# Performance work log

Hardware: AMD Instinct MI355X
Metric: run time of the kernel (lower is better)

The kernel has to match this reference:

```python
import jax, jax.numpy as jnp
import numpy as np

B, T, C, H = 4, 4096, 1024, 16

def setup_inputs() -> dict:
    key = jax.random.key(0)
    k1, k2, k3, k4 = jax.random.split(key, 4)
    return {
        "x": jax.random.normal(k1, (B, T, C), dtype=jnp.float32),
        "W_attn": jax.random.normal(k2, (C, C), dtype=jnp.float32) * 0.02,
        "b_attn": jnp.zeros((C,), dtype=jnp.float32),
        "W_proj": jax.random.normal(k3, (C, C), dtype=jnp.float32) * 0.02,
        "b_proj": jnp.zeros((C,), dtype=jnp.float32),
        "temp": jnp.ones((H, 1), dtype=jnp.float32),
        "n_head": H,
    }

def reference(x, W_attn, b_attn, W_proj, b_proj, temp, n_head):
    Bb, Tt, Cc = x.shape
    D = Cc // n_head
    # c_attn (torch Linear: x @ W.T + b)
    w = x @ W_attn.T + b_attn                         # (B,T,C)
    w = w.reshape(Bb, Tt, n_head, D).transpose(0, 2, 1, 3)  # (B,H,T,D)
    # F.normalize over token axis (dim=-2), eps=1e-12
    norm = jnp.maximum(jnp.sqrt(jnp.sum(w * w, axis=-2, keepdims=True)), 1e-12)
    w_normed = w / norm
    tmp = jnp.sum(w_normed ** 2, axis=-1) * temp      # (B,H,T) * (H,1) -> (B,H,T)
    Pi = jax.nn.softmax(tmp, axis=1)                  # softmax over heads
    Pi_prob = Pi / (jnp.sum(Pi, axis=-1, keepdims=True) + 1e-8)  # (B,H,T)
    dots = jnp.einsum('bht,bhtd->bhd', Pi_prob, w ** 2)          # (B,H,D)
    attn = 1.0 / (1.0 + dots)                         # (B,H,D)
    y = -(w * Pi[..., None]) * attn[:, :, None, :]    # (B,H,T,D)
    y = y.transpose(0, 2, 1, 3).reshape(Bb, Tt, Cc)
    return y @ W_proj.T + b_proj
```

## Files before the change

### kernel.cpp

```cpp
#include <hip/hip_runtime.h>
#include <hip/hip_bf16.h>

#define BB 4
#define TT 4096
#define CC 1024
#define HH 16
#define DD 64

typedef __attribute__((ext_vector_type(8))) short short8;
typedef __attribute__((ext_vector_type(8))) __bf16 bf16x8;
typedef __attribute__((ext_vector_type(4))) float f32x4;

static __device__ __forceinline__ unsigned short f2bf(float f) {
    unsigned int u = __builtin_bit_cast(unsigned int, f);
    unsigned int r = (u + 0x7FFFu + ((u >> 16) & 1u)) >> 16;
    return (unsigned short)r;
}
static __device__ __forceinline__ float bf2f(unsigned short h) {
    return __builtin_bit_cast(float, ((unsigned int)h) << 16);
}

__global__ void k_f32_to_bf16(const float* __restrict__ src,
                              unsigned short* __restrict__ dst, int n4) {
    int i = blockIdx.x * 256 + threadIdx.x;
    if (i >= n4) return;
    float4 v = ((const float4*)src)[i];
    ushort4 o;
    o.x = f2bf(v.x); o.y = f2bf(v.y); o.z = f2bf(v.z); o.w = f2bf(v.w);
    ((ushort4*)dst)[i] = o;
}

#define GBM 256
#define GBN 256
#define GBK 32

static __device__ __forceinline__ void stage_tile32(
    const unsigned short* __restrict__ Gbase, unsigned short* lbase,
    int k0, int K, int wave, int lane)
{
    #pragma unroll
    for (int q = 0; q < 2; ++q) {
        int c = (wave * 2 + q) * 64 + lane;
        int r = c >> 2;
        int j = c & 3;
        int srcj = (j - (r >> 1)) & 3;
        const unsigned short* g = Gbase + (size_t)r * K + k0 + srcj * 8;
        __builtin_amdgcn_global_load_lds(
            (const __attribute__((address_space(1))) void*)g,
            (__attribute__((address_space(3))) void*)(lbase + (wave * 2 + q) * 512),
            16, 0, 0);
    }
}

template<int MODE>
__global__ __launch_bounds__(512, 2)
void k_gemm256(const unsigned short* __restrict__ A,
               const unsigned short* __restrict__ B,
               const float* __restrict__ bias,
               void* __restrict__ Cout,
               float* __restrict__ S,
               int M, int N, int K)
{
    __shared__ unsigned short lds[4][16384];
    const int tid  = threadIdx.x;
    const int wave = tid >> 6;
    const int lane = tid & 63;
    const int wr = wave >> 2;
    const int wc = wave & 3;
    const int fr = lane & 15;
    const int hi = lane >> 4;

    const int wg  = blockIdx.x;
    const int swz = (wg & 7) * 32 + (wg >> 3);
    const int bn  = swz & 3;
    const int bm  = swz >> 2;

    const unsigned short* Abase = A + (size_t)(bm * GBM) * K;
    const unsigned short* Bbase = B + (size_t)(bn * GBN) * K;

    const int nt = K / GBK;

    const int sl   = (hi + (fr >> 1)) & 3;
    const int aoff = (wr * 128 + fr) * 32 + sl * 8;
    const int boff = 8192 + (wc * 64 + fr) * 32 + sl * 8;

    f32x4 acc[8][4] = {};

    stage_tile32(Abase, lds[0],        0,       K, wave, lane);
    stage_tile32(Bbase, lds[0] + 8192, 0,       K, wave, lane);
    stage_tile32(Abase, lds[1],        GBK,     K, wave, lane);
    stage_tile32(Bbase, lds[1] + 8192, GBK,     K, wave, lane);
    stage_tile32(Abase, lds[2],        2 * GBK, K, wave, lane);
    stage_tile32(Bbase, lds[2] + 8192, 2 * GBK, K, wave, lane);
    asm volatile("s_waitcnt vmcnt(8)" ::: "memory");
    __builtin_amdgcn_s_barrier();

    for (int kt = 0; kt < nt; ++kt) {
        const unsigned short* buf = lds[kt & 3];
        unsigned short* sbuf = lds[(kt + 3) & 3];
        int k3 = kt + 3; if (k3 >= nt) k3 = nt - 1;

        short8 af0[4], bf0[4];
        #pragma unroll
        for (int i = 0; i < 4; ++i) af0[i] = *(const short8*)&buf[aoff + i * 512];
        #pragma unroll
        for (int i = 0; i < 4; ++i) bf0[i] = *(const short8*)&buf[boff + i * 512];
        stage_tile32(Abase, sbuf, k3 * GBK, K, wave, lane);
        __builtin_amdgcn_s_barrier();
        asm volatile("s_waitcnt lgkmcnt(0)" ::: "memory");
        __builtin_amdgcn_s_setprio(1);
        #pragma unroll
        for (int mi = 0; mi < 4; ++mi)
            #pragma unroll
            for (int ni = 0; ni < 4; ++ni)
                acc[mi][ni] = __builtin_amdgcn_mfma_f32_16x16x32_bf16(
                    __builtin_bit_cast(bf16x8, af0[mi]),
                    __builtin_bit_cast(bf16x8, bf0[ni]),
                    acc[mi][ni], 0, 0, 0);
        __builtin_amdgcn_s_setprio(0);
        __builtin_amdgcn_s_barrier();

        short8 af1[4], bf1[4];
        #pragma unroll
        for (int i = 0; i < 4; ++i) af1[i] = *(const short8*)&buf[aoff + (4 + i) * 512];
        #pragma unroll
        for (int i = 0; i < 4; ++i) bf1[i] = *(const short8*)&buf[boff + i * 512];
        stage_tile32(Bbase, sbuf + 8192, k3 * GBK, K, wave, lane);
        asm volatile("s_waitcnt vmcnt(8)" ::: "memory");
        __builtin_amdgcn_s_barrier();
        asm volatile("s_waitcnt lgkmcnt(0)" ::: "memory");
        __builtin_amdgcn_s_setprio(1);
        #pragma unroll
        for (int mi = 0; mi < 4; ++mi)
            #pragma unroll
            for (int ni = 0; ni < 4; ++ni)
                acc[4 + mi][ni] = __builtin_amdgcn_mfma_f32_16x16x32_bf16(
                    __builtin_bit_cast(bf16x8, af1[mi]),
                    __builtin_bit_cast(bf16x8, bf1[ni]),
                    acc[4 + mi][ni], 0, 0, 0);
        __builtin_amdgcn_s_setprio(0);
        __builtin_amdgcn_s_barrier();
    }

    __syncthreads();

    const int cg = fr;
    const int rg = hi * 4;
    float* sblk = (float*)&lds[0][0];
    if (MODE == 0) {
        if (tid < GBN) sblk[tid] = 0.f;
        __syncthreads();
    }
    float csum[4] = {};
    #pragma unroll
    for (int mi = 0; mi < 8; ++mi) {
        #pragma unroll
        for (int ni = 0; ni < 4; ++ni) {
            int col = bn * GBN + wc * 64 + ni * 16 + cg;
            float bv = bias[col];
            #pragma unroll
            for (int j = 0; j < 4; ++j) {
                int row = bm * GBM + wr * 128 + mi * 16 + rg + j;
                float v = acc[mi][ni][j] + bv;
                if (MODE == 0) {
                    ((unsigned short*)Cout)[(size_t)row * N + col] = f2bf(v);
                    csum[ni] += v * v;
                } else {
                    ((float*)Cout)[(size_t)row * N + col] = v;
                }
            }
        }
    }
    if (MODE == 0) {
        #pragma unroll
        for (int ni = 0; ni < 4; ++ni)
            atomicAdd(&sblk[wc * 64 + ni * 16 + cg], csum[ni]);
        __syncthreads();
        const int b = bm >> 4;
        if (tid < GBN) atomicAdd(&S[b * CC + bn * GBN + tid], sblk[tid]);
    }
}

__global__ __launch_bounds__(256)
void k_row_softmax(const unsigned short* __restrict__ w16, const float* __restrict__ S,
                   const float* __restrict__ temp,
                   float* __restrict__ Pi, float* __restrict__ dotsU,
                   float* __restrict__ sumPi)
{
    __shared__ float dots_local[CC];
    __shared__ float sPi_local[HH];
    const int tid  = threadIdx.x;
    const int wave = tid >> 6;
    const int lane = tid & 63;
    const int bb   = blockIdx.x >> 7;
    const int tile = blockIdx.x & 127;

    for (int c = tid; c < CC; c += 256) dots_local[c] = 0.f;
    if (tid < HH) sPi_local[tid] = 0.f;
    __syncthreads();

    const int g3 = lane >> 3;
    const int li = lane & 7;

    float inv[2][8], tsc[2];
    #pragma unroll
    for (int q = 0; q < 2; ++q) {
        int c = q * 512 + lane * 8;
        const float4* sp = (const float4*)&S[bb * CC + c];
        float4 s0 = sp[0], s1 = sp[1];
        inv[q][0] = 1.f / fmaxf(s0.x, 1e-24f); inv[q][1] = 1.f / fmaxf(s0.y, 1e-24f);
        inv[q][2] = 1.f / fmaxf(s0.z, 1e-24f); inv[q][3] = 1.f / fmaxf(s0.w, 1e-24f);
        inv[q][4] = 1.f / fmaxf(s1.x, 1e-24f); inv[q][5] = 1.f / fmaxf(s1.y, 1e-24f);
        inv[q][6] = 1.f / fmaxf(s1.z, 1e-24f); inv[q][7] = 1.f / fmaxf(s1.w, 1e-24f);
        tsc[q] = temp[q * 8 + g3];
    }

    float dacc[2][8] = {};
    float sPiAcc[2] = {};

    for (int i = 0; i < 8; ++i) {
        int t = tile * 32 + wave * 8 + i;
        const unsigned short* row = w16 + ((size_t)bb * TT + t) * CC;
        float wf[2][8];
        float pq[2];
        #pragma unroll
        for (int q = 0; q < 2; ++q) {
            short8 v = *(const short8*)&row[q * 512 + lane * 8];
            float s = 0.f;
            #pragma unroll
            for (int j = 0; j < 8; ++j) {
                wf[q][j] = bf2f((unsigned short)v[j]);
                s += wf[q][j] * wf[q][j] * inv[q][j];
            }
            pq[q] = s;
        }
        #pragma unroll
        for (int off = 1; off < 8; off <<= 1) {
            pq[0] += __shfl_xor(pq[0], off);
            pq[1] += __shfl_xor(pq[1], off);
        }
        pq[0] *= tsc[0]; pq[1] *= tsc[1];
        float mx = fmaxf(pq[0], pq[1]);
        mx = fmaxf(mx, __shfl_xor(mx, 8));
        mx = fmaxf(mx, __shfl_xor(mx, 16));
        mx = fmaxf(mx, __shfl_xor(mx, 32));
        float e0 = __expf(pq[0] - mx), e1 = __expf(pq[1] - mx);
        float ss = e0 + e1;
        ss += __shfl_xor(ss, 8);
        ss += __shfl_xor(ss, 16);
        ss += __shfl_xor(ss, 32);
        float rs = 1.f / ss;
        float piv[2] = { e0 * rs, e1 * rs };
        #pragma unroll
        for (int q = 0; q < 2; ++q) {
            #pragma unroll
            for (int j = 0; j < 8; ++j)
                dacc[q][j] += piv[q] * wf[q][j] * wf[q][j];
            if (li == 0) {
                Pi[((size_t)(bb * HH + q * 8 + g3)) * TT + t] = piv[q];
                sPiAcc[q] += piv[q];
            }
        }
    }

    #pragma unroll
    for (int q = 0; q < 2; ++q) {
        int c = q * 512 + lane * 8;
        #pragma unroll
        for (int j = 0; j < 8; ++j)
            atomicAdd(&dots_local[c + j], dacc[q][j]);
        if (li == 0) atomicAdd(&sPi_local[q * 8 + g3], sPiAcc[q]);
    }
    __syncthreads();
    for (int c = tid; c < CC; c += 256) atomicAdd(&dotsU[bb * CC + c], dots_local[c]);
    if (tid < HH) atomicAdd(&sumPi[bb * HH + tid], sPi_local[tid]);
}

__global__ void k_attnscale(const float* __restrict__ dotsU,
                            const float* __restrict__ sumPi,
                            float* __restrict__ attnScale) {
    int i = blockIdx.x * 256 + threadIdx.x;
    if (i >= BB * CC) return;
    int b = i >> 10;
    int h = (i >> 6) & 15;
    float sp = sumPi[b * HH + h] + 1e-8f;
    attnScale[i] = 1.f / (1.f + dotsU[i] / sp);
}

__global__ void k_make_y(unsigned short* __restrict__ wy, const float* __restrict__ Pi,
                         const float* __restrict__ attnScale)
{
    size_t i = (size_t)blockIdx.x * 256 + threadIdx.x;
    size_t flat = i * 8;
    int c = (int)(flat & (CC - 1));
    size_t bt = flat >> 10;
    int t = (int)(bt & (TT - 1));
    int b = (int)(bt >> 12);
    int h = c >> 6;
    float pi = Pi[((size_t)(b * HH + h)) * TT + t];
    short8 wv = *(const short8*)&wy[flat];
    f32x4 a0 = *(const f32x4*)&attnScale[b * CC + c];
    f32x4 a1 = *(const f32x4*)&attnScale[b * CC + c + 4];
    short8 o;
    #pragma unroll
    for (int j = 0; j < 4; ++j) {
        o[j]     = (short)f2bf(-(bf2f((unsigned short)wv[j])     * pi) * a0[j]);
        o[4 + j] = (short)f2bf(-(bf2f((unsigned short)wv[4 + j]) * pi) * a1[j]);
    }
    *(short8*)&wy[flat] = o;
}

extern "C" void kernel_launch(void* const* d_in, const int* in_sizes, int n_in,
                              void* d_out, int out_size, void* d_ws, size_t ws_size,
                              hipStream_t stream) {
    const float* x      = (const float*)d_in[0];
    const float* W_attn = (const float*)d_in[1];
    const float* b_attn = (const float*)d_in[2];
    const float* W_proj = (const float*)d_in[3];
    const float* b_proj = (const float*)d_in[4];
    const float* temp   = (const float*)d_in[5];

    unsigned short* xb = (unsigned short*)d_out;

    char* ws = (char*)d_ws;
    unsigned short* w16  = (unsigned short*)(ws);
    unsigned short* Wa16 = (unsigned short*)(ws + 33554432);
    unsigned short* Wp16 = (unsigned short*)(ws + 35651584);
    float* Pi        = (float*)(ws + 37748736);
    float* S         = (float*)(ws + 38797312);
    float* dotsU     = (float*)(ws + 38813696);
    float* sumPi     = (float*)(ws + 38830080);
    float* attnScale = (float*)(ws + 38830336);

    k_f32_to_bf16<<<dim3(16384), dim3(256), 0, stream>>>(x, xb, 4194304);
    k_f32_to_bf16<<<dim3(1024), dim3(256), 0, stream>>>(W_attn, Wa16, 262144);
    k_f32_to_bf16<<<dim3(1024), dim3(256), 0, stream>>>(W_proj, Wp16, 262144);

    hipMemsetAsync(S, 0, 16384 + 16384 + 256, stream);

    k_gemm256<0><<<dim3(256), dim3(512), 0, stream>>>(
        xb, Wa16, b_attn, w16, S, BB * TT, CC, CC);

    k_row_softmax<<<dim3(512), dim3(256), 0, stream>>>(w16, S, temp, Pi, dotsU, sumPi);

    k_attnscale<<<dim3(16), dim3(256), 0, stream>>>(dotsU, sumPi, attnScale);

    k_make_y<<<dim3(8192), dim3(256), 0, stream>>>(w16, Pi, attnScale);

    k_gemm256<1><<<dim3(256), dim3(512), 0, stream>>>(
        w16, Wp16, b_proj, d_out, nullptr, BB * TT, CC, CC);
}
```

Baseline: 142.8 us.

## Fold per-batch attention scale into projection weights and emit y in softmax pass

The per-(batch, channel) attention scale is folded into per-batch bf16 copies of W_proj, and the row-softmax kernel writes -w*Pi directly over w16. This removes the separate attnscale and make_y passes, the Pi buffer, and one full read/write sweep of the activation tensor. The projection GEMM now picks its batch's weight slice, which adds a small weight-scaling kernel and a larger weight workspace. The GEMM also drops a redundant second LDS load of the B fragments and reuses bf0.

```diff
diff --git a/kernel.cpp b/kernel.cpp
--- a/kernel.cpp
+++ b/kernel.cpp
@@ -74,9 +74,11 @@
     const int swz = (wg & 7) * 32 + (wg >> 3);
     const int bn  = swz & 3;
     const int bm  = swz >> 2;
+    const int b   = bm >> 4;
 
     const unsigned short* Abase = A + (size_t)(bm * GBM) * K;
-    const unsigned short* Bbase = B + (size_t)(bn * GBN) * K;
+    const unsigned short* Bbase = B +
+        ((size_t)((MODE == 1 ? b * N : 0) + bn * GBN)) * K;
 
     const int nt = K / GBK;
 
@@ -120,11 +122,9 @@
         __builtin_amdgcn_s_setprio(0);
         __builtin_amdgcn_s_barrier();
 
-        short8 af1[4], bf1[4];
+        short8 af1[4];
         #pragma unroll
         for (int i = 0; i < 4; ++i) af1[i] = *(const short8*)&buf[aoff + (4 + i) * 512];
-        #pragma unroll
-        for (int i = 0; i < 4; ++i) bf1[i] = *(const short8*)&buf[boff + i * 512];
         stage_tile32(Bbase, sbuf + 8192, k3 * GBK, K, wave, lane);
         asm volatile("s_waitcnt vmcnt(8)" ::: "memory");
         __builtin_amdgcn_s_barrier();
@@ -136,7 +136,7 @@
             for (int ni = 0; ni < 4; ++ni)
                 acc[4 + mi][ni] = __builtin_amdgcn_mfma_f32_16x16x32_bf16(
                     __builtin_bit_cast(bf16x8, af1[mi]),
-                    __builtin_bit_cast(bf16x8, bf1[ni]),
+                    __builtin_bit_cast(bf16x8, bf0[ni]),
                     acc[4 + mi][ni], 0, 0, 0);
         __builtin_amdgcn_s_setprio(0);
         __builtin_amdgcn_s_barrier();
@@ -176,16 +176,14 @@
         for (int ni = 0; ni < 4; ++ni)
             atomicAdd(&sblk[wc * 64 + ni * 16 + cg], csum[ni]);
         __syncthreads();
-        const int b = bm >> 4;
         if (tid < GBN) atomicAdd(&S[b * CC + bn * GBN + tid], sblk[tid]);
     }
 }
 
 __global__ __launch_bounds__(256)
-void k_row_softmax(const unsigned short* __restrict__ w16, const float* __restrict__ S,
+void k_row_softmax(unsigned short* __restrict__ w16, const float* __restrict__ S,
                    const float* __restrict__ temp,
-                   float* __restrict__ Pi, float* __restrict__ dotsU,
-                   float* __restrict__ sumPi)
+                   float* __restrict__ dotsU, float* __restrict__ sumPi)
 {
     __shared__ float dots_local[CC];
     __shared__ float sPi_local[HH];
@@ -220,7 +218,7 @@
 
     for (int i = 0; i < 8; ++i) {
         int t = tile * 32 + wave * 8 + i;
-        const unsigned short* row = w16 + ((size_t)bb * TT + t) * CC;
+        unsigned short* row = w16 + ((size_t)bb * TT + t) * CC;
         float wf[2][8];
         float pq[2];
         #pragma unroll
@@ -253,13 +251,14 @@
         float piv[2] = { e0 * rs, e1 * rs };
         #pragma unroll
         for (int q = 0; q < 2; ++q) {
-            #pragma unroll
-            for (int j = 0; j < 8; ++j)
+            short8 yo;
+            #pragma unroll
+            for (int j = 0; j < 8; ++j) {
                 dacc[q][j] += piv[q] * wf[q][j] * wf[q][j];
-            if (li == 0) {
-                Pi[((size_t)(bb * HH + q * 8 + g3)) * TT + t] = piv[q];
-                sPiAcc[q] += piv[q];
+                yo[j] = (short)f2bf(-wf[q][j] * piv[q]);
             }
+            *(short8*)&row[q * 512 + lane * 8] = yo;
+            if (li == 0) sPiAcc[q] += piv[q];
         }
     }
 
@@ -276,38 +275,27 @@
     if (tid < HH) atomicAdd(&sumPi[bb * HH + tid], sPi_local[tid]);
 }
 
-__global__ void k_attnscale(const float* __restrict__ dotsU,
-                            const float* __restrict__ sumPi,
-                            float* __restrict__ attnScale) {
+__global__ void k_scale_wproj(const float* __restrict__ Wp,
+                              const float* __restrict__ dotsU,
+                              const float* __restrict__ sumPi,
+                              unsigned short* __restrict__ out)
+{
     int i = blockIdx.x * 256 + threadIdx.x;
-    if (i >= BB * CC) return;
-    int b = i >> 10;
-    int h = (i >> 6) & 15;
-    float sp = sumPi[b * HH + h] + 1e-8f;
-    attnScale[i] = 1.f / (1.f + dotsU[i] / sp);
-}
-
-__global__ void k_make_y(unsigned short* __restrict__ wy, const float* __restrict__ Pi,
-                         const float* __restrict__ attnScale)
-{
-    size_t i = (size_t)blockIdx.x * 256 + threadIdx.x;
-    size_t flat = i * 8;
-    int c = (int)(flat & (CC - 1));
-    size_t bt = flat >> 10;
-    int t = (int)(bt & (TT - 1));
-    int b = (int)(bt >> 12);
-    int h = c >> 6;
-    float pi = Pi[((size_t)(b * HH + h)) * TT + t];
-    short8 wv = *(const short8*)&wy[flat];
-    f32x4 a0 = *(const f32x4*)&attnScale[b * CC + c];
-    f32x4 a1 = *(const f32x4*)&attnScale[b * CC + c + 4];
-    short8 o;
-    #pragma unroll
-    for (int j = 0; j < 4; ++j) {
-        o[j]     = (short)f2bf(-(bf2f((unsigned short)wv[j])     * pi) * a0[j]);
-        o[4 + j] = (short)f2bf(-(bf2f((unsigned short)wv[4 + j]) * pi) * a1[j]);
-    }
-    *(short8*)&wy[flat] = o;
+    int bq  = i >> 18;
+    int rem = i & 262143;
+    int n   = rem >> 8;
+    int cg  = (rem & 255) * 4;
+    float4 wv = *(const float4*)&Wp[n * CC + cg];
+    float4 du = *(const float4*)&dotsU[bq * CC + cg];
+    float sp = sumPi[bq * HH + (cg >> 6)] + 1e-8f;
+    float a0 = 1.f / (1.f + du.x / sp);
+    float a1 = 1.f / (1.f + du.y / sp);
+    float a2 = 1.f / (1.f + du.z / sp);
+    float a3 = 1.f / (1.f + du.w / sp);
+    ushort4 o;
+    o.x = f2bf(wv.x * a0); o.y = f2bf(wv.y * a1);
+    o.z = f2bf(wv.z * a2); o.w = f2bf(wv.w * a3);
+    *(ushort4*)&out[((size_t)bq * CC + n) * CC + cg] = o;
 }
 
 extern "C" void kernel_launch(void* const* d_in, const int* in_sizes, int n_in,
@@ -323,30 +311,25 @@
     unsigned short* xb = (unsigned short*)d_out;
 
     char* ws = (char*)d_ws;
-    unsigned short* w16  = (unsigned short*)(ws);
-    unsigned short* Wa16 = (unsigned short*)(ws + 33554432);
-    unsigned short* Wp16 = (unsigned short*)(ws + 35651584);
-    float* Pi        = (float*)(ws + 37748736);
-    float* S         = (float*)(ws + 38797312);
-    float* dotsU     = (float*)(ws + 38813696);
-    float* sumPi     = (float*)(ws + 38830080);
-    float* attnScale = (float*)(ws + 38830336);
+    unsigned short* w16   = (unsigned short*)(ws);
+    unsigned short* Wa16  = (unsigned short*)(ws + 33554432);
+    unsigned short* Wp16b = (unsigned short*)(ws + 35651584);
+    float* S     = (float*)(ws + 44040192);
+    float* dotsU = (float*)(ws + 44056576);
+    float* sumPi = (float*)(ws + 44072960);
 
     k_f32_to_bf16<<<dim3(16384), dim3(256), 0, stream>>>(x, xb, 4194304);
     k_f32_to_bf16<<<dim3(1024), dim3(256), 0, stream>>>(W_attn, Wa16, 262144);
-    k_f32_to_bf16<<<dim3(1024), dim3(256), 0, stream>>>(W_proj, Wp16, 262144);
 
     hipMemsetAsync(S, 0, 16384 + 16384 + 256, stream);
 
     k_gemm256<0><<<dim3(256), dim3(512), 0, stream>>>(
         xb, Wa16, b_attn, w16, S, BB * TT, CC, CC);
 
-    k_row_softmax<<<dim3(512), dim3(256), 0, stream>>>(w16, S, temp, Pi, dotsU, sumPi);
-
-    k_attnscale<<<dim3(16), dim3(256), 0, stream>>>(dotsU, sumPi, attnScale);
-
-    k_make_y<<<dim3(8192), dim3(256), 0, stream>>>(w16, Pi, attnScale);
+    k_row_softmax<<<dim3(512), dim3(256), 0, stream>>>(w16, S, temp, dotsU, sumPi);
+
+    k_scale_wproj<<<dim3(4096), dim3(256), 0, stream>>>(W_proj, dotsU, sumPi, Wp16b);
 
     k_gemm256<1><<<dim3(256), dim3(512), 0, stream>>>(
-        w16, Wp16, b_proj, d_out, nullptr, BB * TT, CC, CC);
-}
+        w16, Wp16b, b_proj, d_out, nullptr, BB * TT, CC, CC);
+}
```

Result: faster. 131.0 us (-8.3%).
